# Performance work log

Hardware: AMD Instinct MI355X
Metric: run time of the kernel (lower is better)

The kernel has to match this reference:

```python
import jax, jax.numpy as jnp
import numpy as np

R_MIN, R_MAX, THETA_MAX = 0.4, 0.99, 6.283185307179586
ORDER = 64  # K = order//2 = 32 pole pairs


def setup_inputs() -> dict:
    key = jax.random.key(0)
    k1, k2, k3, k4, k5 = jax.random.split(key, 5)
    K, D = ORDER // 2, 1024
    u1 = jax.random.uniform(k1, (K, D), dtype=jnp.float32)
    u2 = jax.random.uniform(k2, (K, D), dtype=jnp.float32)
    scale = np.sqrt(2.0 / ORDER).astype(np.float32)
    return {
        "r": R_MIN + (R_MAX - R_MIN) * u1,                         # pole radii
        "theta": THETA_MAX * u2,                                    # pole angles
        "R_re": jax.random.normal(k3, (K, D), dtype=jnp.float32) * scale,
        "R_im": jax.random.normal(k4, (K, D), dtype=jnp.float32) * scale,
        "h_0": jax.random.normal(k5, (1, D), dtype=jnp.float32),
        "L": 2048,
    }


def reference(r, theta, R_re, R_im, h_0, L):
    # poles p = r * exp(i*theta), residues R = R_re + i*R_im; shapes (K, D)
    p = r.astype(jnp.complex64) * jnp.exp(1j * theta.astype(jnp.complex64))
    R = R_re + 1j * R_im                                            # (K, D) complex64
    t = jnp.arange(L - 1, dtype=jnp.float32)[:, None, None]         # (L-1, 1, 1)
    # h[t, d] = Re( sum_k R[k,d] * p[k,d]^t )
    h = jnp.sum(R[None] * p[None] ** t, axis=1).real                # (L-1, D)
    h = jnp.concatenate([h_0, h], axis=0)                           # (L, D)
    return h.T                                                      # (D, L)
```

## Files before the change

kernel.cpp:

```cpp
#include <hip/hip_runtime.h>


#define KP 32
#define KP2 16
#define DD 1024
#define LL 2048
#define INV_2PI 0x1.45f306p-3f

typedef float v2f __attribute__((ext_vector_type(2)));

__global__ __launch_bounds__(256) void modal_filter_kernel(
    const float* __restrict__ r, const float* __restrict__ theta,
    const float* __restrict__ Rre, const float* __restrict__ Rim,
    const float* __restrict__ h0, float* __restrict__ out) {
  const int d = blockIdx.x;
  const int tid = threadIdx.x;

  __shared__ float s_lr[KP];
  __shared__ float s_thr[KP];
  __shared__ float s_qre[KP];
  __shared__ float s_qim[KP];
  __shared__ float s_Rre[KP];
  __shared__ float s_Rim[KP];

  if (tid < KP) {
    const float rv = r[tid * DD + d];
    const float th = theta[tid * DD + d];
    const float lr = __builtin_amdgcn_logf(rv);
    const float thr = th * INV_2PI;
    const float qmag = __builtin_amdgcn_exp2f(256.0f * lr);
    const float qang = __builtin_amdgcn_fractf(256.0f * thr);
    s_lr[tid] = lr;
    s_thr[tid] = thr;
    s_qre[tid] = qmag * __builtin_amdgcn_cosf(qang);
    s_qim[tid] = qmag * __builtin_amdgcn_sinf(qang);
    s_Rre[tid] = Rre[tid * DD + d];
    s_Rim[tid] = Rim[tid * DD + d];
  }
  __syncthreads();

  v2f ZRE[KP2], ZIM[KP2], QRE[KP2], QIM[KP2];
  const float t0 = (float)tid - 1.0f;
#pragma unroll
  for (int kk = 0; kk < KP2; ++kk) {
#pragma unroll
    for (int j = 0; j < 2; ++j) {
      const int k = 2 * kk + j;
      const float mag = __builtin_amdgcn_exp2f(t0 * s_lr[k]);
      const float ang = __builtin_amdgcn_fractf(t0 * s_thr[k]);
      const float c = __builtin_amdgcn_cosf(ang);
      const float s = __builtin_amdgcn_sinf(ang);
      const float wre = mag * c, wim = mag * s;
      ZRE[kk][j] = s_Rre[k] * wre - s_Rim[k] * wim;
      ZIM[kk][j] = s_Rre[k] * wim + s_Rim[k] * wre;
      QRE[kk][j] = s_qre[k];
      QIM[kk][j] = s_qim[k];
    }
  }

  float* outd = out + (size_t)d * LL;
  const float h0d = h0[d];

#pragma unroll
  for (int s = 0; s < 8; ++s) {
    v2f a0 = {0.f, 0.f}, a1 = {0.f, 0.f}, a2 = {0.f, 0.f}, a3 = {0.f, 0.f};
#pragma unroll
    for (int kk = 0; kk < KP2; kk += 4) {
      a0 += ZRE[kk];
      a1 += ZRE[kk + 1];
      a2 += ZRE[kk + 2];
      a3 += ZRE[kk + 3];
    }
    const v2f aa = (a0 + a1) + (a2 + a3);
    const float acc = aa[0] + aa[1];
    const int l = tid + 256 * s;
    outd[l] = (l == 0) ? h0d : acc;
    if (s < 7) {
#pragma unroll
      for (int kk = 0; kk < KP2; ++kk) {
        const v2f nr = ZRE[kk] * QRE[kk] - ZIM[kk] * QIM[kk];
        const v2f ni = ZRE[kk] * QIM[kk] + ZIM[kk] * QRE[kk];
        ZRE[kk] = nr;
        ZIM[kk] = ni;
      }
    }
  }
}

extern "C" void kernel_launch(void* const* d_in, const int* in_sizes, int n_in,
                              void* d_out, int out_size, void* d_ws, size_t ws_size,
                              hipStream_t stream) {
  const float* r     = (const float*)d_in[0];
  const float* theta = (const float*)d_in[1];
  const float* Rre   = (const float*)d_in[2];
  const float* Rim   = (const float*)d_in[3];
  const float* h0    = (const float*)d_in[4];
  float* out = (float*)d_out;

  modal_filter_kernel<<<DD, 256, 0, stream>>>(r, theta, Rre, Rim, h0, out);
}
```

Before: 74.42 us.

## Split per-pole precompute into a separate prep kernel writing a contiguous workspace

Moves the per-pole log/sincos precompute and the strided gathers of r, theta, R into a separate kernel. That kernel writes a per-channel contiguous 192-float record to workspace, which the main kernel reads as uniform (scalar) loads instead of going through shared memory and a barrier. This removes the __syncthreads and the strided 32-lane gather from each main block. The cost is an extra kernel launch and a workspace round trip. It also adds launch_bounds min-blocks of 2, which may limit registers for the 64 v2f arrays.

```diff
diff --git a/kernel.cpp b/kernel.cpp
--- a/kernel.cpp
+++ b/kernel.cpp
@@ -5,39 +5,38 @@
 #define KP2 16
 #define DD 1024
 #define LL 2048
+#define PREPW (6 * KP)
 #define INV_2PI 0x1.45f306p-3f
 
 typedef float v2f __attribute__((ext_vector_type(2)));
 
-__global__ __launch_bounds__(256) void modal_filter_kernel(
+__global__ __launch_bounds__(256) void prep_kernel(
     const float* __restrict__ r, const float* __restrict__ theta,
     const float* __restrict__ Rre, const float* __restrict__ Rim,
-    const float* __restrict__ h0, float* __restrict__ out) {
+    float* __restrict__ prep) {
+  const int d = blockIdx.x * 256 + threadIdx.x;
+  const int k = blockIdx.y;
+  const float rv = r[k * DD + d];
+  const float th = theta[k * DD + d];
+  const float lr = __builtin_amdgcn_logf(rv);
+  const float thr = th * INV_2PI;
+  const float qmag = __builtin_amdgcn_exp2f(256.0f * lr);
+  const float qang = __builtin_amdgcn_fractf(256.0f * thr);
+  float* w = prep + (size_t)d * PREPW;
+  w[k]          = lr;
+  w[KP + k]     = thr;
+  w[2 * KP + k] = qmag * __builtin_amdgcn_cosf(qang);
+  w[3 * KP + k] = qmag * __builtin_amdgcn_sinf(qang);
+  w[4 * KP + k] = Rre[k * DD + d];
+  w[5 * KP + k] = Rim[k * DD + d];
+}
+
+__global__ __launch_bounds__(256, 2) void modal_filter_kernel(
+    const float* __restrict__ prep, const float* __restrict__ h0,
+    float* __restrict__ out) {
   const int d = blockIdx.x;
   const int tid = threadIdx.x;
-
-  __shared__ float s_lr[KP];
-  __shared__ float s_thr[KP];
-  __shared__ float s_qre[KP];
-  __shared__ float s_qim[KP];
-  __shared__ float s_Rre[KP];
-  __shared__ float s_Rim[KP];
-
-  if (tid < KP) {
-    const float rv = r[tid * DD + d];
-    const float th = theta[tid * DD + d];
-    const float lr = __builtin_amdgcn_logf(rv);
-    const float thr = th * INV_2PI;
-    const float qmag = __builtin_amdgcn_exp2f(256.0f * lr);
-    const float qang = __builtin_amdgcn_fractf(256.0f * thr);
-    s_lr[tid] = lr;
-    s_thr[tid] = thr;
-    s_qre[tid] = qmag * __builtin_amdgcn_cosf(qang);
-    s_qim[tid] = qmag * __builtin_amdgcn_sinf(qang);
-    s_Rre[tid] = Rre[tid * DD + d];
-    s_Rim[tid] = Rim[tid * DD + d];
-  }
-  __syncthreads();
+  const float* __restrict__ w = prep + (size_t)d * PREPW;
 
   v2f ZRE[KP2], ZIM[KP2], QRE[KP2], QIM[KP2];
   const float t0 = (float)tid - 1.0f;
@@ -46,15 +45,19 @@
 #pragma unroll
     for (int j = 0; j < 2; ++j) {
       const int k = 2 * kk + j;
-      const float mag = __builtin_amdgcn_exp2f(t0 * s_lr[k]);
-      const float ang = __builtin_amdgcn_fractf(t0 * s_thr[k]);
+      const float lr = w[k];
+      const float thr = w[KP + k];
+      const float mag = __builtin_amdgcn_exp2f(t0 * lr);
+      const float ang = __builtin_amdgcn_fractf(t0 * thr);
       const float c = __builtin_amdgcn_cosf(ang);
       const float s = __builtin_amdgcn_sinf(ang);
       const float wre = mag * c, wim = mag * s;
-      ZRE[kk][j] = s_Rre[k] * wre - s_Rim[k] * wim;
-      ZIM[kk][j] = s_Rre[k] * wim + s_Rim[k] * wre;
-      QRE[kk][j] = s_qre[k];
-      QIM[kk][j] = s_qim[k];
+      const float Rr = w[4 * KP + k];
+      const float Ri = w[5 * KP + k];
+      ZRE[kk][j] = Rr * wre - Ri * wim;
+      ZIM[kk][j] = Rr * wim + Ri * wre;
+      QRE[kk][j] = w[2 * KP + k];
+      QIM[kk][j] = w[3 * KP + k];
     }
   }
 
@@ -96,6 +99,8 @@
   const float* Rim   = (const float*)d_in[3];
   const float* h0    = (const float*)d_in[4];
   float* out = (float*)d_out;
+  float* prep = (float*)d_ws;
 
-  modal_filter_kernel<<<DD, 256, 0, stream>>>(r, theta, Rre, Rim, h0, out);
+  prep_kernel<<<dim3(DD / 256, KP), 256, 0, stream>>>(r, theta, Rre, Rim, prep);
+  modal_filter_kernel<<<DD, 256, 0, stream>>>(prep, h0, out);
 }
```

After: 76.28 us. 2.5% more time.

## Give each thread 8 consecutive outputs and store them as float4 pairs

Applied to the files above, without the earlier changes.

Each thread now produces 8 consecutive time steps (t = 8*tid - 1 onward), advancing by multiplying with the pole p itself instead of p^256. The 8 results are held in registers and written as two float4 stores, replacing eight strided scalar stores. Launch bounds now also request 2 blocks per CU. Using p directly may reduce error accumulation, while wider stores from each thread can lower coalescing efficiency per instruction.

```diff
diff --git a/kernel.cpp b/kernel.cpp
--- a/kernel.cpp
+++ b/kernel.cpp
@@ -9,7 +9,7 @@
 
 typedef float v2f __attribute__((ext_vector_type(2)));
 
-__global__ __launch_bounds__(256) void modal_filter_kernel(
+__global__ __launch_bounds__(256, 2) void modal_filter_kernel(
     const float* __restrict__ r, const float* __restrict__ theta,
     const float* __restrict__ Rre, const float* __restrict__ Rim,
     const float* __restrict__ h0, float* __restrict__ out) {
@@ -18,8 +18,8 @@
 
   __shared__ float s_lr[KP];
   __shared__ float s_thr[KP];
-  __shared__ float s_qre[KP];
-  __shared__ float s_qim[KP];
+  __shared__ float s_pre[KP];
+  __shared__ float s_pim[KP];
   __shared__ float s_Rre[KP];
   __shared__ float s_Rim[KP];
 
@@ -28,19 +28,19 @@
     const float th = theta[tid * DD + d];
     const float lr = __builtin_amdgcn_logf(rv);
     const float thr = th * INV_2PI;
-    const float qmag = __builtin_amdgcn_exp2f(256.0f * lr);
-    const float qang = __builtin_amdgcn_fractf(256.0f * thr);
+    const float ang = __builtin_amdgcn_fractf(thr);
     s_lr[tid] = lr;
     s_thr[tid] = thr;
-    s_qre[tid] = qmag * __builtin_amdgcn_cosf(qang);
-    s_qim[tid] = qmag * __builtin_amdgcn_sinf(qang);
+    s_pre[tid] = rv * __builtin_amdgcn_cosf(ang);
+    s_pim[tid] = rv * __builtin_amdgcn_sinf(ang);
     s_Rre[tid] = Rre[tid * DD + d];
     s_Rim[tid] = Rim[tid * DD + d];
   }
+  const float h0d = h0[d];
   __syncthreads();
 
-  v2f ZRE[KP2], ZIM[KP2], QRE[KP2], QIM[KP2];
-  const float t0 = (float)tid - 1.0f;
+  v2f ZRE[KP2], ZIM[KP2], PRE[KP2], PIM[KP2];
+  const float t0 = 8.0f * (float)tid - 1.0f;
 #pragma unroll
   for (int kk = 0; kk < KP2; ++kk) {
 #pragma unroll
@@ -53,16 +53,14 @@
       const float wre = mag * c, wim = mag * s;
       ZRE[kk][j] = s_Rre[k] * wre - s_Rim[k] * wim;
       ZIM[kk][j] = s_Rre[k] * wim + s_Rim[k] * wre;
-      QRE[kk][j] = s_qre[k];
-      QIM[kk][j] = s_qim[k];
+      PRE[kk][j] = s_pre[k];
+      PIM[kk][j] = s_pim[k];
     }
   }
 
-  float* outd = out + (size_t)d * LL;
-  const float h0d = h0[d];
-
+  float a[8];
 #pragma unroll
-  for (int s = 0; s < 8; ++s) {
+  for (int i = 0; i < 8; ++i) {
     v2f a0 = {0.f, 0.f}, a1 = {0.f, 0.f}, a2 = {0.f, 0.f}, a3 = {0.f, 0.f};
 #pragma unroll
     for (int kk = 0; kk < KP2; kk += 4) {
@@ -72,19 +70,22 @@
       a3 += ZRE[kk + 3];
     }
     const v2f aa = (a0 + a1) + (a2 + a3);
-    const float acc = aa[0] + aa[1];
-    const int l = tid + 256 * s;
-    outd[l] = (l == 0) ? h0d : acc;
-    if (s < 7) {
+    a[i] = aa[0] + aa[1];
+    if (i < 7) {
 #pragma unroll
       for (int kk = 0; kk < KP2; ++kk) {
-        const v2f nr = ZRE[kk] * QRE[kk] - ZIM[kk] * QIM[kk];
-        const v2f ni = ZRE[kk] * QIM[kk] + ZIM[kk] * QRE[kk];
+        const v2f nr = ZRE[kk] * PRE[kk] - ZIM[kk] * PIM[kk];
+        const v2f ni = ZRE[kk] * PIM[kk] + ZIM[kk] * PRE[kk];
         ZRE[kk] = nr;
         ZIM[kk] = ni;
       }
     }
   }
+  if (tid == 0) a[0] = h0d;
+
+  float4* o4 = reinterpret_cast<float4*>(out + (size_t)d * LL);
+  o4[2 * tid]     = make_float4(a[0], a[1], a[2], a[3]);
+  o4[2 * tid + 1] = make_float4(a[4], a[5], a[6], a[7]);
 }
 
 extern "C" void kernel_launch(void* const* d_in, const int* in_sizes, int n_in,
```

New measurement: 73.53 us. No clear change (-1.2%).
